# Performance work log

Hardware: AMD Instinct MI355X
Metric: run time of the kernel (lower is better)

The kernel has to match this reference:

```python
import jax, jax.numpy as jnp
import numpy as np

K = 16          # number of discrete value bins (values in [0, K))
EPOCHS = 200.0  # self.epochs in the module


def _mi_from_joint(joint):
    # sklearn mutual_info_score from a KxK contingency table (natural log)
    n = joint.sum()
    pij = joint / n
    pi = pij.sum(axis=1, keepdims=True)
    pj = pij.sum(axis=0, keepdims=True)
    safe_log = lambda p: jnp.log(jnp.where(p > 0, p, 1.0))
    terms = pij * (safe_log(pij) - safe_log(pi) - safe_log(pj))
    return jnp.where(pij > 0, terms, 0.0).sum()


def _pair_mi(a, b):
    # a, b: int32 vectors of equal length; histogram-based MI
    idx = a * K + b
    joint = jnp.zeros(K * K, jnp.float32).at[idx].add(1.0).reshape(K, K)
    return _mi_from_joint(joint)


def _mi_mask(x):
    # x: (b, t, c, h, w) float with integer values in [0, K)
    b, t, c, h, w = x.shape
    s = x.astype(jnp.int32).transpose(1, 0, 2, 3, 4).reshape(t, b * c, h * w)
    s0 = s[0]
    # global MI between t=0 and each t, over all b*c*h*w samples
    glob = jax.vmap(lambda st: _pair_mi(s0.reshape(-1), st.reshape(-1)))(s)  # (t,)
    # per-spatial-element MI between t=0 and each t, over b*c samples
    ele = jax.vmap(jax.vmap(_pair_mi, in_axes=(1, 1)), in_axes=(None, 0))(s0, s)  # (t, hw)
    mi = ele * glob[:, None]
    mi = mi / mi[0]          # divide every row by row 0 (broadcast over t)
    mi = mi.at[0].set(0.0)
    return mi.reshape(t, h, w)


def setup_inputs() -> dict:
    key = jax.random.key(0)
    k1, k2 = jax.random.split(key)
    b, t, c, h, w = 16, 8, 32, 64, 64
    x = jax.random.randint(k1, (b, t, c, h, w), 0, K).astype(jnp.float32)
    noise = jax.random.uniform(k2, (b, t, c, h, w), dtype=jnp.float32)
    return {"x": x, "noise": noise, "epoch": 50}


def reference(x, noise, epoch):
    mi = _mi_mask(x)                                   # (t, h, w)
    prob = jnp.clip(mi * (epoch / EPOCHS), 0.0, 1.0)
    mask = noise < prob[None, :, None, :, :]           # (b,t,c,h,w)
    return jnp.where(mask, 0.0, x)
```

## Files before the change

### kernel.cpp

```cpp
#include <hip/hip_runtime.h>
#include <math.h>

#define B_   16
#define T_   8
#define C_   32
#define HW_  4096
#define K_   16
#define BC_  (B_*C_)
#define P_BLK 8

typedef unsigned int uint;

__global__ __launch_bounds__(256) void k_pack(const float4* __restrict__ x4,
                                              uint4* __restrict__ packed4,
                                              uint4* __restrict__ glob_hist4) {
  const int tid = threadIdx.x;
  if (blockIdx.x == 0) {
    const uint4 z = make_uint4(0u, 0u, 0u, 0u);
    glob_hist4[tid] = z;
    glob_hist4[tid + 256] = z;
  }
  const int n  = blockIdx.x * 256 + tid;
  const int bc = n >> 10;
  const int p4 = n & 1023;
  const int b  = bc >> 5;
  const int c  = bc & 31;
  uint4 acc = make_uint4(0u, 0u, 0u, 0u);
  #pragma unroll
  for (int t = 0; t < T_; ++t) {
    const float4 xv = x4[((b * T_ + t) * C_ + c) * (HW_ / 4) + p4];
    const int sh = 4 * t;
    acc.x |= ((uint)xv.x) << sh;
    acc.y |= ((uint)xv.y) << sh;
    acc.z |= ((uint)xv.z) << sh;
    acc.w |= ((uint)xv.w) << sh;
  }
  packed4[n] = acc;
}

__global__ __launch_bounds__(512) void k_hist_mi(const uint* __restrict__ packed,
                                                 uint* __restrict__ glob_hist,
                                                 double* __restrict__ ele) {
  __shared__ uint   hist[T_][P_BLK][256];
  __shared__ double logtab[513];

  const int tid = threadIdx.x;
  const int p0  = blockIdx.x * P_BLK;

  for (int i = tid; i < T_ * P_BLK * 256; i += 512) ((uint*)hist)[i] = 0u;
  for (int i = tid; i < 513; i += 512) logtab[i] = (i > 0) ? log((double)i) : 0.0;
  __syncthreads();

  const int lp  = tid & 7;
  const int g   = tid >> 3;
  const int rot = lp * 37;

  uint w[8];
  #pragma unroll
  for (int k = 0; k < 8; ++k)
    w[k] = packed[(g + (k << 6)) * HW_ + p0 + lp];

  #pragma unroll
  for (int k = 0; k < 8; ++k) {
    const uint wk  = w[k];
    const int  a   = (int)(wk & 15u);
    const int  row = a << 4;
    atomicAdd(&hist[0][lp][((row | a) + rot) & 255], 1u);
    #pragma unroll
    for (int t = 1; t < T_; ++t) {
      const int v = (int)((wk >> (4 * t)) & 15u);
      atomicAdd(&hist[t][lp][((row | v) + rot) & 255], 1u);
    }
  }
  __syncthreads();

  for (int i = tid; i < T_ * 256; i += 512) {
    const int t = i >> 8, bin = i & 255;
    uint s = 0;
    #pragma unroll
    for (int p = 0; p < P_BLK; ++p) s += hist[t][p][(bin + p * 37) & 255];
    atomicAdd(&glob_hist[i], s);
  }

  const int wid  = tid >> 6;
  const int lane = tid & 63;
  #pragma unroll
  for (int p = 0; p < P_BLK; ++p) {
    const uint* h = &hist[wid][p][0];
    const int   rr = p * 37;
    double acc = 0.0;
    #pragma unroll
    for (int j0 = 0; j0 < 4; ++j0) {
      const uint cnt = h[((lane << 2) + j0 + rr) & 255];
      acc += (double)cnt * logtab[cnt];
    }
    if (lane < 16) {
      uint r = 0;
      #pragma unroll
      for (int v = 0; v < K_; ++v) r += h[(((lane << 4) | v) + rr) & 255];
      acc -= (double)r * logtab[r];
    } else if (lane < 32) {
      const int v = lane - 16;
      uint col = 0;
      #pragma unroll
      for (int a = 0; a < K_; ++a) col += h[(((a << 4) | v) + rr) & 255];
      acc -= (double)col * logtab[col];
    }
    #pragma unroll
    for (int m = 1; m < 64; m <<= 1) acc += __shfl_xor(acc, m, 64);
    if (lane == 0)
      ele[wid * HW_ + p0 + p] = logtab[512] + acc * (1.0 / 512.0);
  }
}

__global__ __launch_bounds__(256) void k_glob_prob(const uint* __restrict__ glob_hist,
                                                   const double* __restrict__ ele,
                                                   const int* __restrict__ epoch_ptr,
                                                   float* __restrict__ prob) {
  __shared__ double part[256];
  __shared__ double glob[T_];
  const int tid = threadIdx.x;

  if (tid < 128) {
    const int t = tid >> 4, a = tid & 15;
    const uint* h = glob_hist + t * 256 + (a << 4);
    double s = 0.0, r = 0.0;
    #pragma unroll
    for (int v = 0; v < K_; ++v) {
      const double cnt = (double)h[v];
      r += cnt;
      if (cnt > 0.0) s += cnt * log(cnt);
    }
    if (r > 0.0) s -= r * log(r);
    part[tid] = s;
  } else {
    const int t = (tid - 128) >> 4, v = (tid - 128) & 15;
    const uint* h = glob_hist + t * 256 + v;
    double col = 0.0;
    #pragma unroll
    for (int a = 0; a < K_; ++a) col += (double)h[a << 4];
    part[tid] = (col > 0.0) ? -col * log(col) : 0.0;
  }
  __syncthreads();

  if (tid < T_) {
    double term = 0.0;
    #pragma unroll
    for (int i = 0; i < 16; ++i)
      term += part[tid * 16 + i] + part[128 + tid * 16 + i];
    const double n = (double)BC_ * (double)HW_;
    glob[tid] = log(n) + term / n;
  }
  __syncthreads();

  const double escale = (double)(*epoch_ptr) * (1.0 / 200.0);
  #pragma unroll
  for (int k = 0; k < 4; ++k) {
    const int i = blockIdx.x * 1024 + k * 256 + tid;
    const int t = i >> 12;
    const int p = i & (HW_ - 1);
    float pv = 0.0f;
    if (t != 0) {
      const double mi0 = ele[p] * glob[0];
      const double mit = ele[i] * glob[t];
      const double v  = (mit / mi0) * escale;
      pv = fminf(fmaxf((float)v, 0.0f), 1.0f);
    }
    prob[i] = pv;
  }
}

__global__ __launch_bounds__(256) void k_mask(const uint4* __restrict__ packed4,
                                              const float4* __restrict__ n4,
                                              const float* __restrict__ prob,
                                              float4* __restrict__ o4) {
  const int i  = blockIdx.x * 256 + threadIdx.x;
  const int p4 = i & 1023;
  const int tc = i >> 10;
  const int c  = tc & 31;
  const int bt = tc >> 5;
  const int t  = bt & 7;
  const int b  = bt >> 3;
  const uint4 pk = packed4[(((b << 5) | c) << 10) | p4];
  const int sh = 4 * t;
  float4 xv;
  xv.x = (float)((pk.x >> sh) & 15u);
  xv.y = (float)((pk.y >> sh) & 15u);
  xv.z = (float)((pk.z >> sh) & 15u);
  xv.w = (float)((pk.w >> sh) & 15u);
  const float4 pr = ((const float4*)prob)[(t << 10) | p4];
  const float4 nv = n4[i];
  float4 o;
  o.x = (nv.x < pr.x) ? 0.0f : xv.x;
  o.y = (nv.y < pr.y) ? 0.0f : xv.y;
  o.z = (nv.z < pr.z) ? 0.0f : xv.z;
  o.w = (nv.w < pr.w) ? 0.0f : xv.w;
  o4[i] = o;
}

extern "C" void kernel_launch(void* const* d_in, const int* in_sizes, int n_in,
                              void* d_out, int out_size, void* d_ws, size_t ws_size,
                              hipStream_t stream) {
  const float* x     = (const float*)d_in[0];
  const float* noise = (const float*)d_in[1];
  const int*   epoch = (const int*)d_in[2];
  float*       out   = (float*)d_out;

  char* ws = (char*)d_ws;
  uint*   glob_hist = (uint*)ws;
  uint*   packed    = (uint*)(ws + 8192);
  double* ele       = (double*)(ws + 8192 + (size_t)BC_ * HW_ * 4);
  float*  prob      = (float*)((char*)ele + (size_t)T_ * HW_ * 8);

  k_pack<<<(BC_ * HW_ / 4) / 256, 256, 0, stream>>>((const float4*)x,
                                                    (uint4*)packed,
                                                    (uint4*)glob_hist);
  k_hist_mi<<<HW_ / P_BLK, 512, 0, stream>>>(packed, glob_hist, ele);
  k_glob_prob<<<32, 256, 0, stream>>>(glob_hist, ele, epoch, prob);

  const int n4 = (B_ * T_ * C_ * HW_) / 4;
  k_mask<<<n4 / 256, 256, 0, stream>>>((const uint4*)packed,
                                       (const float4*)noise,
                                       prob, (float4*)out);
}
```

Baseline: 208.8 us.

## Pack per-pixel histograms into 16-bit shared counters and serialize MI epilogue

Halves the shared-memory histogram by packing two 16-bit bin counters per 32-bit word, and adds a per-timestep rotation to spread bank conflicts. The smaller LDS footprint and a launch-bounds hint aim to let more blocks be resident per CU. The MI epilogue moves from wave-wide shuffle reductions to one thread per (t, pixel) looping over all 256 bins serially. That serial loop uses only 64 of 512 threads and many registers, so the epilogue may become a long tail.

```diff
diff --git a/kernel.cpp b/kernel.cpp
--- a/kernel.cpp
+++ b/kernel.cpp
@@ -10,6 +10,8 @@
 #define P_BLK 8
 
 typedef unsigned int uint;
+
+__device__ __forceinline__ int rot2_(int t, int lp) { return 37 * lp + 13 * t; }
 
 __global__ __launch_bounds__(256) void k_pack(const float4* __restrict__ x4,
                                               uint4* __restrict__ packed4,
@@ -38,22 +40,21 @@
   packed4[n] = acc;
 }
 
-__global__ __launch_bounds__(512) void k_hist_mi(const uint* __restrict__ packed,
-                                                 uint* __restrict__ glob_hist,
-                                                 double* __restrict__ ele) {
-  __shared__ uint   hist[T_][P_BLK][256];
+__global__ __launch_bounds__(512, 8) void k_hist_mi(const uint* __restrict__ packed,
+                                                    uint* __restrict__ glob_hist,
+                                                    double* __restrict__ ele) {
+  __shared__ uint   histw[T_][P_BLK][128];
   __shared__ double logtab[513];
 
   const int tid = threadIdx.x;
   const int p0  = blockIdx.x * P_BLK;
 
-  for (int i = tid; i < T_ * P_BLK * 256; i += 512) ((uint*)hist)[i] = 0u;
+  for (int i = tid; i < T_ * P_BLK * 128; i += 512) ((uint*)histw)[i] = 0u;
   for (int i = tid; i < 513; i += 512) logtab[i] = (i > 0) ? log((double)i) : 0.0;
   __syncthreads();
 
-  const int lp  = tid & 7;
-  const int g   = tid >> 3;
-  const int rot = lp * 37;
+  const int lp = tid & 7;
+  const int g  = tid >> 3;
 
   uint w[8];
   #pragma unroll
@@ -65,11 +66,15 @@
     const uint wk  = w[k];
     const int  a   = (int)(wk & 15u);
     const int  row = a << 4;
-    atomicAdd(&hist[0][lp][((row | a) + rot) & 255], 1u);
+    {
+      const int rb = ((row | a) + rot2_(0, lp)) & 255;
+      atomicAdd(&histw[0][lp][rb >> 1], 1u << ((rb & 1) << 4));
+    }
     #pragma unroll
     for (int t = 1; t < T_; ++t) {
-      const int v = (int)((wk >> (4 * t)) & 15u);
-      atomicAdd(&hist[t][lp][((row | v) + rot) & 255], 1u);
+      const int v  = (int)((wk >> (4 * t)) & 15u);
+      const int rb = ((row | v) + rot2_(t, lp)) & 255;
+      atomicAdd(&histw[t][lp][rb >> 1], 1u << ((rb & 1) << 4));
     }
   }
   __syncthreads();
@@ -78,38 +83,39 @@
     const int t = i >> 8, bin = i & 255;
     uint s = 0;
     #pragma unroll
-    for (int p = 0; p < P_BLK; ++p) s += hist[t][p][(bin + p * 37) & 255];
+    for (int p = 0; p < P_BLK; ++p) {
+      const int rb = (bin + rot2_(t, p)) & 255;
+      s += (histw[t][p][rb >> 1] >> ((rb & 1) << 4)) & 0xffffu;
+    }
     atomicAdd(&glob_hist[i], s);
   }
 
-  const int wid  = tid >> 6;
-  const int lane = tid & 63;
-  #pragma unroll
-  for (int p = 0; p < P_BLK; ++p) {
-    const uint* h = &hist[wid][p][0];
-    const int   rr = p * 37;
-    double acc = 0.0;
-    #pragma unroll
-    for (int j0 = 0; j0 < 4; ++j0) {
-      const uint cnt = h[((lane << 2) + j0 + rr) & 255];
-      acc += (double)cnt * logtab[cnt];
-    }
-    if (lane < 16) {
+  if (tid < T_ * P_BLK) {
+    const int t   = tid >> 3;
+    const int lpp = tid & 7;
+    const int rr  = rot2_(t, lpp);
+    const uint* h = &histw[t][lpp][0];
+    double term = 0.0;
+    uint col[K_];
+    #pragma unroll
+    for (int v = 0; v < K_; ++v) col[v] = 0u;
+    #pragma unroll
+    for (int a = 0; a < K_; ++a) {
       uint r = 0;
       #pragma unroll
-      for (int v = 0; v < K_; ++v) r += h[(((lane << 4) | v) + rr) & 255];
-      acc -= (double)r * logtab[r];
-    } else if (lane < 32) {
-      const int v = lane - 16;
-      uint col = 0;
-      #pragma unroll
-      for (int a = 0; a < K_; ++a) col += h[(((a << 4) | v) + rr) & 255];
-      acc -= (double)col * logtab[col];
-    }
-    #pragma unroll
-    for (int m = 1; m < 64; m <<= 1) acc += __shfl_xor(acc, m, 64);
-    if (lane == 0)
-      ele[wid * HW_ + p0 + p] = logtab[512] + acc * (1.0 / 512.0);
+      for (int v = 0; v < K_; ++v) {
+        const int  rb  = (((a << 4) | v) + rr) & 255;
+        const uint cnt = (h[rb >> 1] >> ((rb & 1) << 4)) & 0xffffu;
+        r += cnt;
+        col[v] += cnt;
+        term += (double)cnt * logtab[cnt];
+      }
+      term -= (double)r * logtab[r];
+    }
+    #pragma unroll
+    for (int v = 0; v < K_; ++v)
+      term -= (double)col[v] * logtab[col[v]];
+    ele[t * HW_ + p0 + lpp] = logtab[512] + term * (1.0 / 512.0);
   }
 }
 
```

Result: no change. 211.9 us (+1.5%).
